# Kernel tuning notes

Hardware: AMD Instinct MI355X
Metric: run time of the kernel (lower is better)

Reference implementation:

```python
import jax, jax.numpy as jnp
import numpy as np

B, T, E, D = 64, 128, 4, 128
K = 4 * D  # ffn_hidden_dim
AUX_COEF = 0.01


def setup_inputs() -> dict:
    key = jax.random.key(0)
    ks = jax.random.split(key, 7)
    return {
        "x": jax.random.normal(ks[0], (B, T, D), dtype=jnp.float32),
        "expert_w1": jax.random.normal(ks[1], (T, E, D, K), dtype=jnp.float32) * 0.02,
        "expert_b1": jnp.zeros((T, E, K), dtype=jnp.float32),
        "expert_w2": jax.random.normal(ks[2], (T, E, K, D), dtype=jnp.float32) * 0.02,
        "expert_b2": jnp.zeros((T, E, D), dtype=jnp.float32),
        # router_train nn.Linear(D, E): store as [D, E] plus bias [E]
        "router_w": jax.random.normal(ks[3], (D, E), dtype=jnp.float32) * (1.0 / np.sqrt(D)),
        "router_b": jax.random.normal(ks[4], (E,), dtype=jnp.float32) * 0.01,
    }


def reference(x, expert_w1, expert_b1, expert_w2, expert_b2, router_w, router_b):
    # training=True path with use_relu_routing=True
    router_logits = jnp.einsum("btd,de->bte", x, router_w) + router_b  # [B,T,E]
    gates = jax.nn.relu(router_logits)
    gates = gates / (gates.sum(axis=-1, keepdims=True) + 1e-9)

    # per-token, per-expert 2-layer FFN
    hidden = jnp.einsum("btd,tedk->btek", x, expert_w1) + expert_b1  # [B,T,E,K]
    hidden = jax.nn.gelu(hidden, approximate=False)  # torch F.gelu default = exact erf
    expert_outputs = jnp.einsum("btek,tekd->bted", hidden, expert_w2) + expert_b2  # [B,T,E,D]

    output = (expert_outputs * gates[..., None]).sum(axis=2)  # [B,T,D]
    aux_loss = AUX_COEF * gates.sum() / (x.shape[0] * x.shape[1])
    return output, aux_loss
```

## Files before the change

### kernel.cpp

```cpp
#include <hip/hip_runtime.h>
#include <hip/hip_bf16.h>

#define NB 64
#define NT 128
#define NE 4
#define ND 128
#define NK 512

typedef __attribute__((ext_vector_type(8))) short bf16x8;
typedef __attribute__((ext_vector_type(4))) float f32x4;

__device__ __forceinline__ short f2bf(float f) {
    union { float f; unsigned u; } v; v.f = f;
    unsigned r = v.u + 0x7FFFu + ((v.u >> 16) & 1u);
    return (short)(r >> 16);
}

__device__ __forceinline__ float gelu_erf(float x) {
    return 0.5f * x * (1.0f + erff(x * 0.70710678118654752f));
}

__global__ __launch_bounds__(256, 2)
void moe_main(const float* __restrict__ x,
              const float* __restrict__ w1,
              const float* __restrict__ b1,
              const float* __restrict__ w2,
              const float* __restrict__ b2,
              const float* __restrict__ rw,
              const float* __restrict__ rb,
              float* __restrict__ out,
              float* __restrict__ ws,
              int use_ws)
{
    const int blk  = blockIdx.x;
    const int t    = blk >> 2;
    const int e    = blk & 3;
    const int tid  = threadIdx.x;
    const int lane = tid & 63;
    const int wave = tid >> 6;
    const int l15  = lane & 15;
    const int l4   = lane >> 4;

    __shared__ short Hs[NB][NK + 8];
    __shared__ float gate_s[NB];

    if (tid < NB) {
        const int b = tid;
        const float* xr = x + (b * NT + t) * ND;
        float l0 = rb[0], l1 = rb[1], l2 = rb[2], l3 = rb[3];
        #pragma unroll 8
        for (int d = 0; d < ND; ++d) {
            const float xv = xr[d];
            const float* w = rw + d * NE;
            l0 += xv * w[0]; l1 += xv * w[1]; l2 += xv * w[2]; l3 += xv * w[3];
        }
        l0 = fmaxf(l0, 0.f); l1 = fmaxf(l1, 0.f); l2 = fmaxf(l2, 0.f); l3 = fmaxf(l3, 0.f);
        const float s   = l0 + l1 + l2 + l3;
        const float inv = 1.f / (s + 1e-9f);
        const float ge  = (e == 0) ? l0 : (e == 1) ? l1 : (e == 2) ? l2 : l3;
        gate_s[b] = ge * inv;
        if (e == 0) {
            float aux = s * inv;
            #pragma unroll
            for (int off = 32; off > 0; off >>= 1) aux += __shfl_down(aux, off);
            if (lane == 0) atomicAdd(out + NB * NT * ND, aux * (0.01f / (NB * NT)));
        }
    }
    __syncthreads();

    const float* W1 = w1 + (size_t)((t * NE + e) * ND) * NK;
    const float* B1 = b1 + (t * NE + e) * NK;
    const int n0 = wave * 128;

    f32x4 acc[4][8];
    #pragma unroll
    for (int m = 0; m < 4; ++m)
        #pragma unroll
        for (int n = 0; n < 8; ++n) acc[m][n] = (f32x4){0.f, 0.f, 0.f, 0.f};

    #pragma unroll
    for (int ks = 0; ks < 4; ++ks) {
        const int d0 = ks * 32 + l4 * 8;
        bf16x8 afr[4];
        #pragma unroll
        for (int m = 0; m < 4; ++m) {
            const int b = m * 16 + l15;
            const float* xp = x + (b * NT + t) * ND + d0;
            const float4 u = *(const float4*)(xp);
            const float4 v = *(const float4*)(xp + 4);
            bf16x8 a;
            a[0] = f2bf(u.x); a[1] = f2bf(u.y); a[2] = f2bf(u.z); a[3] = f2bf(u.w);
            a[4] = f2bf(v.x); a[5] = f2bf(v.y); a[6] = f2bf(v.z); a[7] = f2bf(v.w);
            afr[m] = a;
        }
        #pragma unroll
        for (int nt = 0; nt < 8; ++nt) {
            const int n = n0 + nt * 16 + l15;
            const float* wp = W1 + (size_t)d0 * NK + n;
            bf16x8 bfr;
            #pragma unroll
            for (int j = 0; j < 8; ++j) bfr[j] = f2bf(wp[(size_t)j * NK]);
            #pragma unroll
            for (int m = 0; m < 4; ++m)
                acc[m][nt] = __builtin_amdgcn_mfma_f32_16x16x32_bf16(afr[m], bfr, acc[m][nt], 0, 0, 0);
        }
    }

    #pragma unroll
    for (int nt = 0; nt < 8; ++nt) {
        const int n = n0 + nt * 16 + l15;
        const float bb = B1[n];
        #pragma unroll
        for (int m = 0; m < 4; ++m) {
            const int row = m * 16 + l4 * 4;
            #pragma unroll
            for (int r = 0; r < 4; ++r) {
                const float h = acc[m][nt][r] + bb;
                Hs[row + r][n] = f2bf(gelu_erf(h));
            }
        }
    }
    __syncthreads();

    const float* W2 = w2 + (size_t)((t * NE + e) * NK) * ND;
    const float* B2 = b2 + (t * NE + e) * ND;
    const int c0 = wave * 32;

    f32x4 acc2[4][2];
    #pragma unroll
    for (int m = 0; m < 4; ++m)
        #pragma unroll
        for (int n = 0; n < 2; ++n) acc2[m][n] = (f32x4){0.f, 0.f, 0.f, 0.f};

    #pragma unroll 4
    for (int ks = 0; ks < 16; ++ks) {
        const int k0 = ks * 32 + l4 * 8;
        bf16x8 afr[4];
        #pragma unroll
        for (int m = 0; m < 4; ++m)
            afr[m] = *(const bf16x8*)(&Hs[m * 16 + l15][k0]);
        #pragma unroll
        for (int nt = 0; nt < 2; ++nt) {
            const int c = c0 + nt * 16 + l15;
            const float* wp = W2 + (size_t)k0 * ND + c;
            bf16x8 bfr;
            #pragma unroll
            for (int j = 0; j < 8; ++j) bfr[j] = f2bf(wp[(size_t)j * ND]);
            #pragma unroll
            for (int m = 0; m < 4; ++m)
                acc2[m][nt] = __builtin_amdgcn_mfma_f32_16x16x32_bf16(afr[m], bfr, acc2[m][nt], 0, 0, 0);
        }
    }

    #pragma unroll
    for (int nt = 0; nt < 2; ++nt) {
        const int c = c0 + nt * 16 + l15;
        const float bb = B2[c];
        #pragma unroll
        for (int m = 0; m < 4; ++m) {
            #pragma unroll
            for (int r = 0; r < 4; ++r) {
                const int b = m * 16 + l4 * 4 + r;
                const float v = (acc2[m][nt][r] + bb) * gate_s[b];
                if (use_ws) ws[(size_t)(e * NB * NT + b * NT + t) * ND + c] = v;
                else        atomicAdd(out + (size_t)(b * NT + t) * ND + c, v);
            }
        }
    }
}

__global__ __launch_bounds__(256)
void moe_reduce(const float* __restrict__ ws, float* __restrict__ out)
{
    const int i = blockIdx.x * blockDim.x + threadIdx.x;
    const int stride = NB * NT * ND / 4;
    const float4* w = (const float4*)ws;
    const float4 a = w[i];
    const float4 b = w[i + stride];
    const float4 c = w[i + 2 * stride];
    const float4 d = w[i + 3 * stride];
    float4 r;
    r.x = a.x + b.x + c.x + d.x;
    r.y = a.y + b.y + c.y + d.y;
    r.z = a.z + b.z + c.z + d.z;
    r.w = a.w + b.w + c.w + d.w;
    ((float4*)out)[i] = r;
}

extern "C" void kernel_launch(void* const* d_in, const int* in_sizes, int n_in,
                              void* d_out, int out_size, void* d_ws, size_t ws_size,
                              hipStream_t stream) {
    const float* x  = (const float*)d_in[0];
    const float* w1 = (const float*)d_in[1];
    const float* b1 = (const float*)d_in[2];
    const float* w2 = (const float*)d_in[3];
    const float* b2 = (const float*)d_in[4];
    const float* rw = (const float*)d_in[5];
    const float* rb = (const float*)d_in[6];
    float* out = (float*)d_out;

    const size_t ws_need = (size_t)NE * NB * NT * ND * sizeof(float);
    const int use_ws = (ws_size >= ws_need) ? 1 : 0;

    if (use_ws) {
        hipMemsetAsync(out + NB * NT * ND, 0, sizeof(float), stream);
    } else {
        hipMemsetAsync(d_out, 0, (size_t)(NB * NT * ND + 1) * sizeof(float), stream);
    }

    moe_main<<<NT * NE, 256, 0, stream>>>(x, w1, b1, w2, b2, rw, rb, out,
                                          (float*)d_ws, use_ws);
    if (use_ws) {
        moe_reduce<<<(NB * NT * ND / 4) / 256, 256, 0, stream>>>((const float*)d_ws, out);
    }
}
```

Measured before the change: 76.28 us.

## Use 512-thread blocks, stage x in LDS, prefetch weights, atomic-reduce experts

Doubles block size to eight waves so each wave computes a smaller N slice in both GEMMs. The x tile is loaded once into shared memory as bf16 instead of being re-read and converted per wave. Weight loads are software-prefetched four steps ahead in a register ring. The workspace-plus-reduce-kernel path is replaced by direct atomicAdd into a zeroed output, which removes the second launch but adds atomic contention across the four experts. The bf16 conversion now uses the library intrinsic, and shared memory is reused between the X and H buffers.

```diff
diff --git a/kernel.cpp b/kernel.cpp
--- a/kernel.cpp
+++ b/kernel.cpp
@@ -8,19 +8,33 @@
 #define NK 512
 
 typedef __attribute__((ext_vector_type(8))) short bf16x8;
+typedef __attribute__((ext_vector_type(4))) short bf16x4;
 typedef __attribute__((ext_vector_type(4))) float f32x4;
 
 __device__ __forceinline__ short f2bf(float f) {
-    union { float f; unsigned u; } v; v.f = f;
-    unsigned r = v.u + 0x7FFFu + ((v.u >> 16) & 1u);
-    return (short)(r >> 16);
+    union { __hip_bfloat16 b; short s; } u;
+    u.b = __float2bfloat16(f);
+    return u.s;
+}
+
+__device__ __forceinline__ bf16x8 cvt8(const float* f) {
+    bf16x8 r;
+    #pragma unroll
+    for (int j = 0; j < 8; ++j) r[j] = f2bf(f[j]);
+    return r;
+}
+
+__device__ __forceinline__ bf16x4 cvt4(float4 f) {
+    bf16x4 r;
+    r[0] = f2bf(f.x); r[1] = f2bf(f.y); r[2] = f2bf(f.z); r[3] = f2bf(f.w);
+    return r;
 }
 
 __device__ __forceinline__ float gelu_erf(float x) {
     return 0.5f * x * (1.0f + erff(x * 0.70710678118654752f));
 }
 
-__global__ __launch_bounds__(256, 2)
+__global__ __launch_bounds__(512, 4)
 void moe_main(const float* __restrict__ x,
               const float* __restrict__ w1,
               const float* __restrict__ b1,
@@ -28,25 +42,43 @@
               const float* __restrict__ b2,
               const float* __restrict__ rw,
               const float* __restrict__ rb,
-              float* __restrict__ out,
-              float* __restrict__ ws,
-              int use_ws)
+              float* __restrict__ out)
 {
-    const int blk  = blockIdx.x;
-    const int t    = blk >> 2;
-    const int e    = blk & 3;
+    const int bid  = blockIdx.x;
+    const int t    = bid >> 2;
+    const int e    = bid & 3;
     const int tid  = threadIdx.x;
     const int lane = tid & 63;
     const int wave = tid >> 6;
     const int l15  = lane & 15;
     const int l4   = lane >> 4;
 
-    __shared__ short Hs[NB][NK + 8];
-    __shared__ float gate_s[NB];
+    __shared__ __align__(16) char smem[66816];
+    short* Hs     = (short*)smem;
+    short* Xs     = (short*)smem;
+    float* gate_s = (float*)(smem + 66560);
+
+    {
+        float4 xv[4];
+        #pragma unroll
+        for (int q = 0; q < 4; ++q) {
+            const int f   = q * 512 + tid;
+            const int row = f >> 5;
+            const int c4  = f & 31;
+            xv[q] = *(const float4*)(x + (size_t)(row * NT + t) * ND + c4 * 4);
+        }
+        #pragma unroll
+        for (int q = 0; q < 4; ++q) {
+            const int f   = q * 512 + tid;
+            const int row = f >> 5;
+            const int c4  = f & 31;
+            *(bf16x4*)&Xs[row * 136 + c4 * 4] = cvt4(xv[q]);
+        }
+    }
 
     if (tid < NB) {
         const int b = tid;
-        const float* xr = x + (b * NT + t) * ND;
+        const float* xr = x + (size_t)(b * NT + t) * ND;
         float l0 = rb[0], l1 = rb[1], l2 = rb[2], l3 = rb[3];
         #pragma unroll 8
         for (int d = 0; d < ND; ++d) {
@@ -63,51 +95,59 @@
             float aux = s * inv;
             #pragma unroll
             for (int off = 32; off > 0; off >>= 1) aux += __shfl_down(aux, off);
-            if (lane == 0) atomicAdd(out + NB * NT * ND, aux * (0.01f / (NB * NT)));
+            if (lane == 0)
+                atomicAdd(out + NB * NT * ND, aux * (0.01f / (NB * NT)));
         }
     }
     __syncthreads();
 
     const float* W1 = w1 + (size_t)((t * NE + e) * ND) * NK;
     const float* B1 = b1 + (t * NE + e) * NK;
-    const int n0 = wave * 128;
-
-    f32x4 acc[4][8];
+    const int n0 = wave * 64;
+
+    f32x4 acc[4][4];
     #pragma unroll
     for (int m = 0; m < 4; ++m)
         #pragma unroll
-        for (int n = 0; n < 8; ++n) acc[m][n] = (f32x4){0.f, 0.f, 0.f, 0.f};
-
-    #pragma unroll
-    for (int ks = 0; ks < 4; ++ks) {
-        const int d0 = ks * 32 + l4 * 8;
+        for (int n = 0; n < 4; ++n) acc[m][n] = (f32x4){0.f, 0.f, 0.f, 0.f};
+
+    {
+        const float* wbase = W1 + (size_t)(l4 * 8) * NK + n0 + l15;
+        float wbuf[4][8];
+        #pragma unroll
+        for (int q = 0; q < 4; ++q) {
+            const float* wp = wbase + q * 16;
+            #pragma unroll
+            for (int j = 0; j < 8; ++j) wbuf[q][j] = wp[(size_t)j * NK];
+        }
+
         bf16x8 afr[4];
         #pragma unroll
-        for (int m = 0; m < 4; ++m) {
-            const int b = m * 16 + l15;
-            const float* xp = x + (b * NT + t) * ND + d0;
-            const float4 u = *(const float4*)(xp);
-            const float4 v = *(const float4*)(xp + 4);
-            bf16x8 a;
-            a[0] = f2bf(u.x); a[1] = f2bf(u.y); a[2] = f2bf(u.z); a[3] = f2bf(u.w);
-            a[4] = f2bf(v.x); a[5] = f2bf(v.y); a[6] = f2bf(v.z); a[7] = f2bf(v.w);
-            afr[m] = a;
-        }
-        #pragma unroll
-        for (int nt = 0; nt < 8; ++nt) {
-            const int n = n0 + nt * 16 + l15;
-            const float* wp = W1 + (size_t)d0 * NK + n;
-            bf16x8 bfr;
-            #pragma unroll
-            for (int j = 0; j < 8; ++j) bfr[j] = f2bf(wp[(size_t)j * NK]);
+        for (int p = 0; p < 16; ++p) {
+            const int ks = p >> 2, nt = p & 3;
+            if (nt == 0) {
+                const int d0 = ks * 32 + l4 * 8;
+                #pragma unroll
+                for (int m = 0; m < 4; ++m)
+                    afr[m] = *(const bf16x8*)&Xs[(m * 16 + l15) * 136 + d0];
+            }
+            const bf16x8 bfr = cvt8(wbuf[p & 3]);
+            if (p < 12) {
+                const int p4 = p + 4;
+                const int ks4 = p4 >> 2, nt4 = p4 & 3;
+                const float* wp = wbase + (size_t)(ks4 * 32) * NK + nt4 * 16;
+                #pragma unroll
+                for (int j = 0; j < 8; ++j) wbuf[p4 & 3][j] = wp[(size_t)j * NK];
+            }
             #pragma unroll
             for (int m = 0; m < 4; ++m)
                 acc[m][nt] = __builtin_amdgcn_mfma_f32_16x16x32_bf16(afr[m], bfr, acc[m][nt], 0, 0, 0);
         }
     }
-
-    #pragma unroll
-    for (int nt = 0; nt < 8; ++nt) {
+    __syncthreads();
+
+    #pragma unroll
+    for (int nt = 0; nt < 4; ++nt) {
         const int n = n0 + nt * 16 + l15;
         const float bb = B1[n];
         #pragma unroll
@@ -115,8 +155,8 @@
             const int row = m * 16 + l4 * 4;
             #pragma unroll
             for (int r = 0; r < 4; ++r) {
-                const float h = acc[m][nt][r] + bb;
-                Hs[row + r][n] = f2bf(gelu_erf(h));
+                const float hh = acc[m][nt][r] + bb;
+                Hs[(row + r) * 520 + n] = f2bf(gelu_erf(hh));
             }
         }
     }
@@ -124,67 +164,55 @@
 
     const float* W2 = w2 + (size_t)((t * NE + e) * NK) * ND;
     const float* B2 = b2 + (t * NE + e) * ND;
-    const int c0 = wave * 32;
-
-    f32x4 acc2[4][2];
-    #pragma unroll
-    for (int m = 0; m < 4; ++m)
-        #pragma unroll
-        for (int n = 0; n < 2; ++n) acc2[m][n] = (f32x4){0.f, 0.f, 0.f, 0.f};
-
-    #pragma unroll 4
-    for (int ks = 0; ks < 16; ++ks) {
-        const int k0 = ks * 32 + l4 * 8;
-        bf16x8 afr[4];
-        #pragma unroll
-        for (int m = 0; m < 4; ++m)
-            afr[m] = *(const bf16x8*)(&Hs[m * 16 + l15][k0]);
-        #pragma unroll
-        for (int nt = 0; nt < 2; ++nt) {
-            const int c = c0 + nt * 16 + l15;
-            const float* wp = W2 + (size_t)k0 * ND + c;
-            bf16x8 bfr;
-            #pragma unroll
-            for (int j = 0; j < 8; ++j) bfr[j] = f2bf(wp[(size_t)j * ND]);
+    const int c0 = wave * 16;
+
+    f32x4 acc2[4];
+    #pragma unroll
+    for (int m = 0; m < 4; ++m) acc2[m] = (f32x4){0.f, 0.f, 0.f, 0.f};
+
+    {
+        const float* w2base = W2 + (size_t)(l4 * 8) * ND + c0 + l15;
+        float wb2[4][8];
+        #pragma unroll
+        for (int q = 0; q < 4; ++q) {
+            const float* wp = w2base + (size_t)(q * 32) * ND;
+            #pragma unroll
+            for (int j = 0; j < 8; ++j) wb2[q][j] = wp[(size_t)j * ND];
+        }
+
+        bf16x8 a2[4];
+        #pragma unroll
+        for (int p = 0; p < 16; ++p) {
+            const int k0 = p * 32 + l4 * 8;
             #pragma unroll
             for (int m = 0; m < 4; ++m)
-                acc2[m][nt] = __builtin_amdgcn_mfma_f32_16x16x32_bf16(afr[m], bfr, acc2[m][nt], 0, 0, 0);
-        }
-    }
-
-    #pragma unroll
-    for (int nt = 0; nt < 2; ++nt) {
-        const int c = c0 + nt * 16 + l15;
+                a2[m] = *(const bf16x8*)(&Hs[(m * 16 + l15) * 520 + k0]);
+            const bf16x8 bfr = cvt8(wb2[p & 3]);
+            if (p < 12) {
+                const int ks4 = p + 4;
+                const float* wp = w2base + (size_t)(ks4 * 32) * ND;
+                #pragma unroll
+                for (int j = 0; j < 8; ++j) wb2[(p + 4) & 3][j] = wp[(size_t)j * ND];
+            }
+            #pragma unroll
+            for (int m = 0; m < 4; ++m)
+                acc2[m] = __builtin_amdgcn_mfma_f32_16x16x32_bf16(a2[m], bfr, acc2[m], 0, 0, 0);
+        }
+    }
+
+    {
+        const int c = c0 + l15;
         const float bb = B2[c];
         #pragma unroll
         for (int m = 0; m < 4; ++m) {
             #pragma unroll
             for (int r = 0; r < 4; ++r) {
                 const int b = m * 16 + l4 * 4 + r;
-                const float v = (acc2[m][nt][r] + bb) * gate_s[b];
-                if (use_ws) ws[(size_t)(e * NB * NT + b * NT + t) * ND + c] = v;
-                else        atomicAdd(out + (size_t)(b * NT + t) * ND + c, v);
-            }
-        }
-    }
-}
-
-__global__ __launch_bounds__(256)
-void moe_reduce(const float* __restrict__ ws, float* __restrict__ out)
-{
-    const int i = blockIdx.x * blockDim.x + threadIdx.x;
-    const int stride = NB * NT * ND / 4;
-    const float4* w = (const float4*)ws;
-    const float4 a = w[i];
-    const float4 b = w[i + stride];
-    const float4 c = w[i + 2 * stride];
-    const float4 d = w[i + 3 * stride];
-    float4 r;
-    r.x = a.x + b.x + c.x + d.x;
-    r.y = a.y + b.y + c.y + d.y;
-    r.z = a.z + b.z + c.z + d.z;
-    r.w = a.w + b.w + c.w + d.w;
-    ((float4*)out)[i] = r;
+                const float v = (acc2[m][r] + bb) * gate_s[b];
+                atomicAdd(out + (size_t)(b * NT + t) * ND + c, v);
+            }
+        }
+    }
 }
 
 extern "C" void kernel_launch(void* const* d_in, const int* in_sizes, int n_in,
@@ -199,18 +227,6 @@
     const float* rb = (const float*)d_in[6];
     float* out = (float*)d_out;
 
-    const size_t ws_need = (size_t)NE * NB * NT * ND * sizeof(float);
-    const int use_ws = (ws_size >= ws_need) ? 1 : 0;
-
-    if (use_ws) {
-        hipMemsetAsync(out + NB * NT * ND, 0, sizeof(float), stream);
-    } else {
-        hipMemsetAsync(d_out, 0, (size_t)(NB * NT * ND + 1) * sizeof(float), stream);
-    }
-
-    moe_main<<<NT * NE, 256, 0, stream>>>(x, w1, b1, w2, b2, rw, rb, out,
-                                          (float*)d_ws, use_ws);
-    if (use_ws) {
-        moe_reduce<<<(NB * NT * ND / 4) / 256, 256, 0, stream>>>((const float*)d_ws, out);
-    }
-}
+    hipMemsetAsync(d_out, 0, (size_t)(NB * NT * ND + 1) * sizeof(float), stream);
+    moe_main<<<NT * NE, 512, 0, stream>>>(x, w1, b1, w2, b2, rw, rb, out);
+}
```

After: 66.67 us. -12.6%, faster.
